# Performance work log

Hardware: AMD Instinct MI355X
Metric: run time of the kernel (lower is better)

## Reference

```python
import jax, jax.numpy as jnp
import numpy as np

N, E, F_IN = 50000, 800000, 64
HID, HEADS = 64, 4
NEG_SLOPE = 0.2  # PyG GATConv default leaky_relu slope
BN_EPS = 1e-5
NEG_BIG = -1e9
# (in_dim, heads, out_per_head) for each of the 3 layers
DIMS = [(F_IN, HEADS, HID), (HID * HEADS, HEADS, HID), (HID * HEADS, 1, 2)]


def setup_inputs() -> dict:
    key = jax.random.key(0)
    kx, ke, ka, kp = jax.random.split(key, 4)
    inp = {
        "x": jax.random.normal(kx, (N, F_IN), jnp.float32),
        "edge_index": jax.random.randint(ke, (2, E), 0, N),
        "edge_attr": jax.random.randint(ka, (E, 1), 0, 4),
    }
    pk = jax.random.split(kp, 6 * len(DIMS))
    c = 0
    for i, (din, h, dout) in enumerate(DIMS):
        # 4 edge-type-specific GAT convs, params stacked along leading axis
        inp[f"W{i}"] = jax.random.normal(pk[c], (4, din, h * dout), jnp.float32) / np.float32(np.sqrt(din)); c += 1
        inp[f"As{i}"] = jax.random.normal(pk[c], (4, h, dout), jnp.float32) * 0.1; c += 1
        inp[f"Ad{i}"] = jax.random.normal(pk[c], (4, h, dout), jnp.float32) * 0.1; c += 1
        inp[f"cb{i}"] = jnp.zeros((4, h * dout), jnp.float32)
        inp[f"skW{i}"] = jax.random.normal(pk[c], (din, h * dout), jnp.float32) / np.float32(np.sqrt(din)); c += 1
        inp[f"skb{i}"] = jnp.zeros((h * dout,), jnp.float32)
        inp[f"bng{i}"] = jnp.ones((din,), jnp.float32)
        inp[f"bnb{i}"] = jnp.zeros((din,), jnp.float32)
    return inp


def batch_norm(x, gamma, beta):
    # training-mode BatchNorm1d over the node axis (biased variance, as in torch)
    m = x.mean(axis=0)
    v = x.var(axis=0)
    return (x - m) * jax.lax.rsqrt(v + BN_EPS) * gamma + beta


def gat_conv(x, W, a_src, a_dst, bias, src, dst, mask, n):
    # Standard GAT attention restricted to edges of one class (mask) --
    # equivalent to running the conv on the boolean-indexed subgraph.
    heads, dout = a_src.shape
    h = (x @ W).reshape(n, heads, dout)                      # [N,H,D]
    es = jnp.einsum('nhd,hd->nh', h, a_src)                  # [N,H]
    ed = jnp.einsum('nhd,hd->nh', h, a_dst)                  # [N,H]
    e = jax.nn.leaky_relu(es[src] + ed[dst], NEG_SLOPE)      # [E,H]
    e = jnp.where(mask[:, None], e, NEG_BIG)
    emax = jax.ops.segment_max(e, dst, num_segments=n)       # [N,H]
    emax = jnp.where(jnp.isfinite(emax), emax, 0.0)          # empty segments -> -inf
    a = jnp.exp(e - emax[dst])
    a = jnp.where(mask[:, None], a, 0.0)
    denom = jax.ops.segment_sum(a, dst, num_segments=n)      # [N,H]
    msg = jax.ops.segment_sum(a[:, :, None] * h[src], dst, num_segments=n)  # [N,H,D]
    out = msg / jnp.where(denom > 0, denom, 1.0)[:, :, None]
    return out.reshape(n, heads * dout) + bias


def reference(x, edge_index, edge_attr,
              W0, As0, Ad0, cb0, skW0, skb0, bng0, bnb0,
              W1, As1, Ad1, cb1, skW1, skb1, bng1, bnb1,
              W2, As2, Ad2, cb2, skW2, skb2, bng2, bnb2):
    src, dst = edge_index[0], edge_index[1]
    edge_class = edge_attr[:, -1]
    n = x.shape[0]
    layers = [
        (W0, As0, Ad0, cb0, skW0, skb0, bng0, bnb0),
        (W1, As1, Ad1, cb1, skW1, skb1, bng1, bnb1),
        (W2, As2, Ad2, cb2, skW2, skb2, bng2, bnb2),
    ]
    for (W, As, Ad, cb, skW, skb, g, b) in layers:
        x = batch_norm(x, g, b)
        x0 = x @ skW + skb
        for j in range(4):  # fixed small loop over edge types
            x0 = x0 + gat_conv(x, W[j], As[j], Ad[j], cb[j], src, dst,
                               edge_class == j, n)
        x = jax.nn.relu(x0)
    return x
```

## Files before the change

kernel.cpp:

```cpp
#include <hip/hip_runtime.h>
#include <cstddef>
#include <cstdint>

#define NN 50000
#define EE 800000

constexpr float BN_EPS   = 1e-5f;
constexpr float NEGSLOPE = 0.2f;

typedef short s16x8 __attribute__((ext_vector_type(8)));
typedef float f32x4 __attribute__((ext_vector_type(4)));
typedef unsigned short u16x4 __attribute__((ext_vector_type(4)));

__device__ __forceinline__ unsigned short f2bf(float f) {
  unsigned int u = __float_as_uint(f);
  unsigned int r = (u + 0x7fffu + ((u >> 16) & 1u)) >> 16;
  return (unsigned short)r;
}
__device__ __forceinline__ float bf2f(unsigned short u) {
  return __uint_as_float(((unsigned int)u) << 16);
}
__device__ __forceinline__ float leaky(float e) { return e >= 0.f ? e : NEGSLOPE * e; }
__device__ __forceinline__ float sel4(float v0, float v1, float v2, float v3, int h) {
  float r = v0;
  r = (h == 1) ? v1 : r;
  r = (h == 2) ? v2 : r;
  r = (h == 3) ? v3 : r;
  return r;
}
__device__ __forceinline__ void gl_lds16(const unsigned short* g, unsigned short* l) {
  __builtin_amdgcn_global_load_lds(
      (const __attribute__((address_space(1))) unsigned int*)(g),
      (__attribute__((address_space(3))) unsigned int*)(l), 16, 0, 0);
}

__global__ void count_edges_k(const int* __restrict__ ei, const int* __restrict__ cls,
                              int* __restrict__ counts) {
  int e = blockIdx.x * 256 + threadIdx.x;
  if (e >= EE) return;
  int dst = ei[EE + e];
  int c   = cls[e];
  atomicAdd(&counts[dst * 4 + c], 1);
}

__global__ void scan_local_k(const int* __restrict__ counts, int* __restrict__ rs,
                             int* __restrict__ bsum, int n) {
  __shared__ int sh[256];
  int b = blockIdx.x, t = threadIdx.x;
  int base = b * 1024;
  int v[4];
  #pragma unroll
  for (int q = 0; q < 4; q++) {
    int i = base + t * 4 + q;
    v[q] = (i < n) ? counts[i] : 0;
  }
  v[1] += v[0]; v[2] += v[1]; v[3] += v[2];
  sh[t] = v[3];
  __syncthreads();
  for (int off = 1; off < 256; off <<= 1) {
    int x = (t >= off) ? sh[t - off] : 0;
    __syncthreads();
    sh[t] += x;
    __syncthreads();
  }
  int prev = (t > 0) ? sh[t - 1] : 0;
  #pragma unroll
  for (int q = 0; q < 4; q++) {
    int i = base + t * 4 + q;
    if (i < n) rs[i + 1] = prev + v[q];
  }
  if (t == 255) bsum[b] = sh[255];
}

__global__ void scan_bsum_k(int* __restrict__ bsum, int nb) {
  __shared__ int sh[256];
  int t = threadIdx.x;
  sh[t] = (t < nb) ? bsum[t] : 0;
  __syncthreads();
  for (int off = 1; off < 256; off <<= 1) {
    int x = (t >= off) ? sh[t - off] : 0;
    __syncthreads();
    sh[t] += x;
    __syncthreads();
  }
  if (t < nb) bsum[t] = (t > 0) ? sh[t - 1] : 0;
}

__global__ void scan_add_k(int* __restrict__ rs, const int* __restrict__ bsum, int n) {
  int b = blockIdx.x, t = threadIdx.x;
  int off = bsum[b];
  #pragma unroll
  for (int q = 0; q < 4; q++) {
    int i = b * 1024 + t * 4 + q;
    if (i < n) rs[i + 1] += off;
  }
  if (b == 0 && t == 0) rs[0] = 0;
}

__global__ void fill_edges_k(const int* __restrict__ ei, const int* __restrict__ cls,
                             const int* __restrict__ rs, int* __restrict__ cursor,
                             int* __restrict__ ssrc) {
  int e = blockIdx.x * 256 + threadIdx.x;
  if (e >= EE) return;
  int dst = ei[EE + e];
  int c   = cls[e];
  int bin = dst * 4 + c;
  int pos = rs[bin] + atomicAdd(&cursor[bin], 1);
  ssrc[pos] = ei[e];
}

template <bool RELU>
__global__ void bn_stats_k(const float* __restrict__ x, float* __restrict__ sums,
                           int din, int total4) {
  __shared__ float ls[512];
  int t = threadIdx.x;
  for (int i = t; i < 2 * din; i += 256) ls[i] = 0.f;
  __syncthreads();
  int dmask = din - 1;
  int start = blockIdx.x * 256 + t;
  int c0 = (start * 4) & dmask;
  float s[4] = {0.f, 0.f, 0.f, 0.f};
  float ss[4] = {0.f, 0.f, 0.f, 0.f};
  for (int idx = start; idx < total4; idx += gridDim.x * 256) {
    float4 v = ((const float4*)x)[idx];
    float a0 = RELU ? fmaxf(v.x, 0.f) : v.x;
    float a1 = RELU ? fmaxf(v.y, 0.f) : v.y;
    float a2 = RELU ? fmaxf(v.z, 0.f) : v.z;
    float a3 = RELU ? fmaxf(v.w, 0.f) : v.w;
    s[0] += a0; s[1] += a1; s[2] += a2; s[3] += a3;
    ss[0] += a0 * a0; ss[1] += a1 * a1; ss[2] += a2 * a2; ss[3] += a3 * a3;
  }
  #pragma unroll
  for (int q = 0; q < 4; q++) {
    atomicAdd(&ls[c0 + q], s[q]);
    atomicAdd(&ls[din + c0 + q], ss[q]);
  }
  __syncthreads();
  for (int i = t; i < 2 * din; i += 256) atomicAdd(&sums[i], ls[i]);
}

__global__ void bn_finalize_k(const float* __restrict__ sums, const float* __restrict__ g,
                              const float* __restrict__ b, float* __restrict__ scale,
                              float* __restrict__ shift, int din,
                              const float* __restrict__ skb, const float* __restrict__ cb,
                              float* __restrict__ skbe, int hd) {
  int i = threadIdx.x;
  if (i < din) {
    float m  = sums[i] / (float)NN;
    float v  = sums[din + i] / (float)NN - m * m;
    float r  = rsqrtf(v + BN_EPS);
    float sc = r * g[i];
    scale[i] = sc;
    shift[i] = b[i] - m * sc;
  }
  if (i < hd) {
    float acc = skb[i];
    #pragma unroll
    for (int j = 0; j < 4; j++) acc += cb[j * hd + i];
    skbe[i] = acc;
  }
}

template <bool RELU>
__global__ void bn_apply_bf16_k(const float* __restrict__ x, unsigned short* __restrict__ xn,
                                const float* __restrict__ scale, const float* __restrict__ shift,
                                int dmask, int total4) {
  for (int i = blockIdx.x * 256 + threadIdx.x; i < total4; i += gridDim.x * 256) {
    float4 v = ((const float4*)x)[i];
    int c0 = (i * 4) & dmask;
    if (RELU) {
      v.x = fmaxf(v.x, 0.f); v.y = fmaxf(v.y, 0.f);
      v.z = fmaxf(v.z, 0.f); v.w = fmaxf(v.w, 0.f);
    }
    u16x4 o;
    o[0] = f2bf(v.x * scale[c0 + 0] + shift[c0 + 0]);
    o[1] = f2bf(v.y * scale[c0 + 1] + shift[c0 + 1]);
    o[2] = f2bf(v.z * scale[c0 + 2] + shift[c0 + 2]);
    o[3] = f2bf(v.w * scale[c0 + 3] + shift[c0 + 3]);
    ((u16x4*)xn)[i] = o;
  }
}

__global__ void conv_weights_k(const float* __restrict__ skW0, const float* __restrict__ W0,
                               const float* __restrict__ skW1, const float* __restrict__ W1,
                               unsigned short* __restrict__ wt) {
  int o = blockIdx.x * 256 + threadIdx.x;
  if (o >= 409600) return;
  float v;
  if (o < 16384) {
    int n = o >> 6, k = o & 63;
    v = skW0[k * 256 + n];
  } else if (o < 81920) {
    int w = o - 16384; int j = w >> 14; w &= 16383;
    int n = w >> 6, k = w & 63;
    v = W0[j * 16384 + k * 256 + n];
  } else if (o < 147456) {
    int w = o - 81920;
    int n = w >> 8, k = w & 255;
    v = skW1[k * 256 + n];
  } else {
    int w = o - 147456; int j = w >> 16; w &= 65535;
    int n = w >> 8, k = w & 255;
    v = W1[j * 65536 + k * 256 + n];
  }
  wt[o] = f2bf(v);
}

__global__ __launch_bounds__(256) void gemm_bf16_k(
    const unsigned short* __restrict__ A,
    const unsigned short* __restrict__ Bt,
    const float* __restrict__ bias,
    float* __restrict__ Cf,
    unsigned short* __restrict__ Cb,
    const float* __restrict__ asrc,
    const float* __restrict__ adst,
    float* __restrict__ es4,
    float* __restrict__ ed4,
    int M, int K, int N, int strideBt, long long strideC) {
  __shared__ unsigned short As[128 * 32];
  __shared__ unsigned short Bs[128 * 32];
  int z = blockIdx.z;
  Bt += (size_t)z * strideBt;
  int tid  = threadIdx.x;
  int lane = tid & 63;
  int w    = tid >> 6;
  int lm = lane & 15, lq = lane >> 4;
  int row0 = blockIdx.y * 128, col0 = blockIdx.x * 128;
  int wr = (w >> 1) * 64, wc = (w & 1) * 64;
  f32x4 acc[4][4];
  #pragma unroll
  for (int i = 0; i < 4; i++)
    #pragma unroll
    for (int j = 0; j < 4; j++) acc[i][j] = {0.f, 0.f, 0.f, 0.f};
  int ldsbase = (tid & ~63) * 16;

  for (int k0 = 0; k0 < K; k0 += 32) {
    #pragma unroll
    for (int r = 0; r < 2; r++) {
      int ia = r * 256 + tid;
      int arow = row0 + (ia >> 2);
      if (arow >= M) arow = M - 1;
      const unsigned short* ga = A + (size_t)arow * K + k0 + (ia & 3) * 8;
      gl_lds16(ga, (unsigned short*)((char*)As + r * 4096 + ldsbase));
      int bcol = col0 + (ia >> 2);
      const unsigned short* gb = Bt + (size_t)bcol * K + k0 + (ia & 3) * 8;
      gl_lds16(gb, (unsigned short*)((char*)Bs + r * 4096 + ldsbase));
    }
    __syncthreads();
    s16x8 af[4], bfr[4];
    #pragma unroll
    for (int i = 0; i < 4; i++)
      af[i] = *(const s16x8*)&As[(wr + i * 16 + lm) * 32 + lq * 8];
    #pragma unroll
    for (int j = 0; j < 4; j++)
      bfr[j] = *(const s16x8*)&Bs[(wc + j * 16 + lm) * 32 + lq * 8];
    #pragma unroll
    for (int i = 0; i < 4; i++)
      #pragma unroll
      for (int j = 0; j < 4; j++)
        acc[i][j] = __builtin_amdgcn_mfma_f32_16x16x32_bf16(af[i], bfr[j], acc[i][j], 0, 0, 0);
    __syncthreads();
  }

  #pragma unroll
  for (int i = 0; i < 4; i++) {
    #pragma unroll
    for (int j = 0; j < 4; j++) {
      int c = col0 + wc + j * 16 + lm;
      #pragma unroll
      for (int rg = 0; rg < 4; rg++) {
        int r = row0 + wr + i * 16 + lq * 4 + rg;
        if (r < M) {
          float v = acc[i][j][rg];
          if (Cf) {
            if (bias) v += bias[c];
            Cf[(size_t)r * N + c] = v;
          } else {
            Cb[(size_t)z * strideC + (size_t)r * N + c] = f2bf(v);
          }
        }
      }
    }
  }

  if (es4) {
    int hh = (col0 + wc) >> 6;
    float as_v[4], ad_v[4];
    #pragma unroll
    for (int j = 0; j < 4; j++) {
      int gcol = col0 + wc + j * 16 + lm;
      as_v[j] = asrc[z * 256 + gcol];
      ad_v[j] = adst[z * 256 + gcol];
    }
    #pragma unroll
    for (int i = 0; i < 4; i++) {
      #pragma unroll
      for (int rg = 0; rg < 4; rg++) {
        float se = 0.f, sd = 0.f;
        #pragma unroll
        for (int j = 0; j < 4; j++) {
          se += acc[i][j][rg] * as_v[j];
          sd += acc[i][j][rg] * ad_v[j];
        }
        #pragma unroll
        for (int off = 8; off > 0; off >>= 1) {
          se += __shfl_xor(se, off);
          sd += __shfl_xor(sd, off);
        }
        int r = row0 + wr + i * 16 + lq * 4 + rg;
        if (r < M) {
          if (lm == 0) es4[((size_t)z * NN + r) * 4 + hh] = se;
          if (lm == 1) ed4[((size_t)z * NN + r) * 4 + hh] = sd;
        }
      }
    }
  }
}

__global__ __launch_bounds__(256) void gat_agg4_fused_k(
    const unsigned short* __restrict__ hfeat4,
    const float* __restrict__ es4,
    const float* __restrict__ ed4,
    const int* __restrict__ rs, const int* __restrict__ ssrc,
    float* __restrict__ x0) {
  int node = blockIdx.x * 4 + (threadIdx.x >> 6);
  int lane = threadIdx.x & 63;
  if (node >= NN) return;
  int r0 = rs[node * 4 + 0], r1 = rs[node * 4 + 1], r2 = rs[node * 4 + 2],
      r3 = rs[node * 4 + 3], r4 = rs[node * 4 + 4];
  if (r0 == r4) return;
  int h = lane >> 4;

  float acc[4][4];
  float den[4];
  #pragma unroll
  for (int j = 0; j < 4; j++) {
    den[j] = 0.f;
    #pragma unroll
    for (int q = 0; q < 4; q++) acc[j][q] = 0.f;
  }

  #pragma unroll
  for (int j = 0; j < 4; j++) {
    int beg = (j == 0) ? r0 : (j == 1) ? r1 : (j == 2) ? r2 : r3;
    int end = (j == 0) ? r1 : (j == 1) ? r2 : (j == 2) ? r3 : r4;
    if (beg == end) continue;
    const float4 edv = *(const float4*)(ed4 + ((size_t)j * NN + node) * 4);
    const unsigned short* hfj = hfeat4 + (size_t)j * NN * 256;
    const float* esj = es4 + (size_t)j * NN * 4;
    for (int base = beg; base < end; base += 64) {
      int idx = base + lane;
      int s = -1;
      float w0 = 0.f, w1 = 0.f, w2 = 0.f, w3 = 0.f;
      if (idx < end) {
        s = ssrc[idx];
        float4 ev = *(const float4*)(esj + (size_t)s * 4);
        w0 = __expf(leaky(ev.x + edv.x));
        w1 = __expf(leaky(ev.y + edv.y));
        w2 = __expf(leaky(ev.z + edv.z));
        w3 = __expf(leaky(ev.w + edv.w));
      }
      int n_e = min(64, end - base);
      #pragma unroll 2
      for (int i = 0; i < n_e; i++) {
        int si   = __shfl(s, i);
        float b0 = __shfl(w0, i), b1 = __shfl(w1, i),
              b2 = __shfl(w2, i), b3 = __shfl(w3, i);
        float wh = sel4(b0, b1, b2, b3, h);
        u16x4 f = *(const u16x4*)(hfj + (size_t)si * 256 + lane * 4);
        acc[j][0] += wh * bf2f(f[0]);
        acc[j][1] += wh * bf2f(f[1]);
        acc[j][2] += wh * bf2f(f[2]);
        acc[j][3] += wh * bf2f(f[3]);
        den[j] += wh;
      }
    }
  }

  float4* xp = (float4*)(x0 + (size_t)node * 256 + lane * 4);
  float4 cur = *xp;
  #pragma unroll
  for (int j = 0; j < 4; j++) {
    if (den[j] > 0.f) {
      float inv = 1.f / den[j];
      cur.x += acc[j][0] * inv;
      cur.y += acc[j][1] * inv;
      cur.z += acc[j][2] * inv;
      cur.w += acc[j][3] * inv;
    }
  }
  *xp = cur;
}

__global__ __launch_bounds__(256) void layer2_fused_k(
    const unsigned short* __restrict__ xa,
    const float* __restrict__ skW,
    const float* __restrict__ W,
    const float* __restrict__ As2,
    const float* __restrict__ Ad2,
    const float* __restrict__ skbe,
    float* __restrict__ x02,
    float* __restrict__ hf2,
    float* __restrict__ es2,
    float* __restrict__ ed2) {
  __shared__ float wsk[256][2];
  __shared__ float wcl[4][256][2];
  int t = threadIdx.x;
  wsk[t][0] = skW[t * 2];
  wsk[t][1] = skW[t * 2 + 1];
  #pragma unroll
  for (int j = 0; j < 4; j++) {
    wcl[j][t][0] = W[j * 512 + t * 2];
    wcl[j][t][1] = W[j * 512 + t * 2 + 1];
  }
  __syncthreads();
  int node = blockIdx.x * 256 + t;
  if (node >= NN) return;
  const unsigned short* row = xa + (size_t)node * 256;
  float s0 = 0.f, s1 = 0.f;
  float h[4][2] = {};
  for (int k = 0; k < 256; k += 4) {
    u16x4 xr = *(const u16x4*)(row + k);
    #pragma unroll
    for (int q = 0; q < 4; q++) {
      float xv = bf2f(xr[q]);
      s0 += xv * wsk[k + q][0];
      s1 += xv * wsk[k + q][1];
      #pragma unroll
      for (int j = 0; j < 4; j++) {
        h[j][0] += xv * wcl[j][k + q][0];
        h[j][1] += xv * wcl[j][k + q][1];
      }
    }
  }
  x02[(size_t)node * 2]     = s0 + skbe[0];
  x02[(size_t)node * 2 + 1] = s1 + skbe[1];
  #pragma unroll
  for (int j = 0; j < 4; j++) {
    hf2[((size_t)j * NN + node) * 2]     = h[j][0];
    hf2[((size_t)j * NN + node) * 2 + 1] = h[j][1];
    es2[(size_t)j * NN + node] = h[j][0] * As2[j * 2] + h[j][1] * As2[j * 2 + 1];
    ed2[(size_t)j * NN + node] = h[j][0] * Ad2[j * 2] + h[j][1] * Ad2[j * 2 + 1];
  }
}

__global__ __launch_bounds__(256) void gat_agg2_fused_k(
    const float* __restrict__ hf2,
    const float* __restrict__ es2,
    const float* __restrict__ ed2,
    const int* __restrict__ rs, const int* __restrict__ ssrc,
    float* __restrict__ x0) {
  int node = blockIdx.x * 4 + (threadIdx.x >> 6);
  int lane = threadIdx.x & 63;
  if (node >= NN) return;
  float add0 = 0.f, add1 = 0.f;
  #pragma unroll
  for (int j = 0; j < 4; j++) {
    int beg = rs[node * 4 + j], end = rs[node * 4 + j + 1];
    if (beg == end) continue;
    float edv = ed2[(size_t)j * NN + node];
    float nw = 0.f, n0 = 0.f, n1 = 0.f;
    for (int idx = beg + lane; idx < end; idx += 64) {
      int s = ssrc[idx];
      float w = __expf(leaky(es2[(size_t)j * NN + s] + edv));
      float2 f = *(const float2*)(hf2 + ((size_t)j * NN + s) * 2);
      nw += w; n0 += w * f.x; n1 += w * f.y;
    }
    #pragma unroll
    for (int off = 32; off > 0; off >>= 1) {
      nw += __shfl_xor(nw, off);
      n0 += __shfl_xor(n0, off);
      n1 += __shfl_xor(n1, off);
    }
    float inv = 1.f / nw;
    add0 += n0 * inv;
    add1 += n1 * inv;
  }
  if (lane == 0) {
    x0[(size_t)node * 2]     += add0;
    x0[(size_t)node * 2 + 1] += add1;
  }
}

__global__ void relu_k(const float* __restrict__ in, float* __restrict__ out, int n) {
  for (int i = blockIdx.x * 256 + threadIdx.x; i < n; i += gridDim.x * 256)
    out[i] = fmaxf(in[i], 0.f);
}

extern "C" void kernel_launch(void* const* d_in, const int* in_sizes, int n_in,
                              void* d_out, int out_size, void* d_ws, size_t ws_size,
                              hipStream_t stream) {
  (void)in_sizes; (void)n_in; (void)out_size; (void)ws_size;
  const float* x_in = (const float*)d_in[0];
  const int* ei  = (const int*)d_in[1];
  const int* cls = (const int*)d_in[2];
  const float *W[3], *Asr[3], *Adr[3], *cb[3], *skW[3], *skb[3], *bng[3], *bnb[3];
  for (int i = 0; i < 3; i++) {
    int b = 3 + 8 * i;
    W[i]   = (const float*)d_in[b + 0];
    Asr[i] = (const float*)d_in[b + 1];
    Adr[i] = (const float*)d_in[b + 2];
    cb[i]  = (const float*)d_in[b + 3];
    skW[i] = (const float*)d_in[b + 4];
    skb[i] = (const float*)d_in[b + 5];
    bng[i] = (const float*)d_in[b + 6];
    bnb[i] = (const float*)d_in[b + 7];
  }
  float* out = (float*)d_out;

  char* wsp = (char*)d_ws;
  auto alloc = [&](size_t bytes) {
    char* p = wsp;
    wsp += (bytes + 255) & ~(size_t)255;
    return p;
  };
  float*          x0     = (float*)alloc((size_t)NN * 256 * 4);
  unsigned short* xa     = (unsigned short*)alloc((size_t)NN * 256 * 2);
  unsigned short* hfeat4 = (unsigned short*)alloc((size_t)4 * NN * 256 * 2);
  float*          hf2    = (float*)alloc((size_t)4 * NN * 2 * 4);
  float*          es4    = (float*)alloc((size_t)4 * NN * 4 * 4);
  float*          ed4    = (float*)alloc((size_t)4 * NN * 4 * 4);
  float*          stats  = (float*)alloc(512 * 4);
  float*          scale  = (float*)alloc(256 * 4);
  float*          shift  = (float*)alloc(256 * 4);
  float*          skbe   = (float*)alloc(256 * 4);
  unsigned short* wt     = (unsigned short*)alloc((size_t)409600 * 2);
  int*            counts = (int*)alloc((size_t)NN * 4 * 4);
  int*            rs     = (int*)alloc(((size_t)NN * 4 + 1) * 4);
  int*            cursor = (int*)alloc((size_t)NN * 4 * 4);
  int*            bsum   = (int*)alloc(256 * 4);
  int*            ssrc   = (int*)alloc((size_t)EE * 4);

  hipMemsetAsync(counts, 0, (size_t)NN * 4 * 4, stream);
  hipMemsetAsync(cursor, 0, (size_t)NN * 4 * 4, stream);
  count_edges_k<<<(EE + 255) / 256, 256, 0, stream>>>(ei, cls, counts);
  scan_local_k<<<196, 256, 0, stream>>>(counts, rs, bsum, NN * 4);
  scan_bsum_k<<<1, 256, 0, stream>>>(bsum, 196);
  scan_add_k<<<196, 256, 0, stream>>>(rs, bsum, NN * 4);
  fill_edges_k<<<(EE + 255) / 256, 256, 0, stream>>>(ei, cls, rs, cursor, ssrc);

  conv_weights_k<<<1600, 256, 0, stream>>>(skW[0], W[0], skW[1], W[1], wt);

  for (int L = 0; L < 2; L++) {
    int din = (L == 0) ? 64 : 256;
    int total4 = NN * din / 4;
    const float* lin = (L == 0) ? x_in : x0;
    hipMemsetAsync(stats, 0, 512 * 4, stream);
    if (L == 0) {
      bn_stats_k<false><<<512, 256, 0, stream>>>(lin, stats, din, total4);
    } else {
      bn_stats_k<true><<<512, 256, 0, stream>>>(lin, stats, din, total4);
    }
    bn_finalize_k<<<1, 256, 0, stream>>>(stats, bng[L], bnb[L], scale, shift, din,
                                         skb[L], cb[L], skbe, 256);
    if (L == 0) {
      bn_apply_bf16_k<false><<<1024, 256, 0, stream>>>(lin, xa, scale, shift, din - 1, total4);
    } else {
      bn_apply_bf16_k<true><<<1024, 256, 0, stream>>>(lin, xa, scale, shift, din - 1, total4);
    }

    const unsigned short* wsk = wt + (L ? 81920 : 0);
    dim3 ggs(2, (NN + 127) / 128, 1);
    gemm_bf16_k<<<ggs, 256, 0, stream>>>(xa, wsk, skbe, x0, nullptr,
                                         nullptr, nullptr, nullptr, nullptr,
                                         NN, din, 256, 0, 0);
    const unsigned short* wcv = wt + (L ? 147456 : 16384);
    int sB = L ? 65536 : 16384;
    dim3 ggc(2, (NN + 127) / 128, 4);
    gemm_bf16_k<<<ggc, 256, 0, stream>>>(xa, wcv, nullptr, nullptr, hfeat4,
                                         Asr[L], Adr[L], es4, ed4,
                                         NN, din, 256, sB, (long long)NN * 256);
    gat_agg4_fused_k<<<(NN + 3) / 4, 256, 0, stream>>>(hfeat4, es4, ed4, rs, ssrc, x0);
  }

  hipMemsetAsync(stats, 0, 512 * 4, stream);
  bn_stats_k<true><<<512, 256, 0, stream>>>(x0, stats, 256, NN * 64);
  bn_finalize_k<<<1, 256, 0, stream>>>(stats, bng[2], bnb[2], scale, shift, 256,
                                       skb[2], cb[2], skbe, 2);
  bn_apply_bf16_k<true><<<1024, 256, 0, stream>>>(x0, xa, scale, shift, 255, NN * 64);
  layer2_fused_k<<<(NN + 255) / 256, 256, 0, stream>>>(xa, skW[2], W[2], Asr[2], Adr[2],
                                                       skbe, x0, hf2, es4, ed4);
  gat_agg2_fused_k<<<(NN + 3) / 4, 256, 0, stream>>>(hf2, es4, ed4, rs, ssrc, x0);
  relu_k<<<64, 256, 0, stream>>>(x0, out, NN * 2);
}
```

Measured before the change: 758.9 us.

## Merge skip and conv GEMMs, single-pass aggregation for low-degree nodes, fuse final relu

The skip GEMM and the four per-class conv GEMMs now run as one launch with a five-slice grid. The layer-0/1 aggregation kernel gains a fast path for nodes with at most 64 incoming edges. That path computes all edge weights at once, normalises them per class with a wave prefix scan, stages them in LDS, and then runs one gather loop over all classes instead of four serial loops. The last aggregation writes relu(x02 + msg) directly, which removes the separate relu kernel. The intent is to cut launch count, tail effects and per-class loop overhead, at the cost of more complex code and extra shuffles.

Result: faster. 692.2 us (-8.8%).

```diff
diff --git a/kernel.cpp b/kernel.cpp
--- a/kernel.cpp
+++ b/kernel.cpp
@@ -208,19 +208,20 @@
 
 __global__ __launch_bounds__(256) void gemm_bf16_k(
     const unsigned short* __restrict__ A,
-    const unsigned short* __restrict__ Bt,
-    const float* __restrict__ bias,
-    float* __restrict__ Cf,
-    unsigned short* __restrict__ Cb,
+    const unsigned short* __restrict__ BtSk,
+    const unsigned short* __restrict__ BtCv,
+    const float* __restrict__ skbe,
+    float* __restrict__ x0,
+    unsigned short* __restrict__ hfeat4,
     const float* __restrict__ asrc,
     const float* __restrict__ adst,
     float* __restrict__ es4,
     float* __restrict__ ed4,
-    int M, int K, int N, int strideBt, long long strideC) {
+    int M, int K) {
   __shared__ unsigned short As[128 * 32];
   __shared__ unsigned short Bs[128 * 32];
   int z = blockIdx.z;
-  Bt += (size_t)z * strideBt;
+  const unsigned short* Bt = (z == 0) ? BtSk : BtCv + (size_t)(z - 1) * 256 * K;
   int tid  = threadIdx.x;
   int lane = tid & 63;
   int w    = tid >> 6;
@@ -262,35 +263,39 @@
     __syncthreads();
   }
 
-  #pragma unroll
-  for (int i = 0; i < 4; i++) {
-    #pragma unroll
-    for (int j = 0; j < 4; j++) {
-      int c = col0 + wc + j * 16 + lm;
+  if (z == 0) {
+    #pragma unroll
+    for (int i = 0; i < 4; i++)
       #pragma unroll
-      for (int rg = 0; rg < 4; rg++) {
-        int r = row0 + wr + i * 16 + lq * 4 + rg;
-        if (r < M) {
-          float v = acc[i][j][rg];
-          if (Cf) {
-            if (bias) v += bias[c];
-            Cf[(size_t)r * N + c] = v;
-          } else {
-            Cb[(size_t)z * strideC + (size_t)r * N + c] = f2bf(v);
-          }
+      for (int j = 0; j < 4; j++) {
+        int c = col0 + wc + j * 16 + lm;
+        #pragma unroll
+        for (int rg = 0; rg < 4; rg++) {
+          int r = row0 + wr + i * 16 + lq * 4 + rg;
+          if (r < M) x0[(size_t)r * 256 + c] = acc[i][j][rg] + skbe[c];
         }
       }
-    }
-  }
-
-  if (es4) {
+  } else {
+    int cl = z - 1;
+    unsigned short* Cb = hfeat4 + (size_t)cl * NN * 256;
+    #pragma unroll
+    for (int i = 0; i < 4; i++)
+      #pragma unroll
+      for (int j = 0; j < 4; j++) {
+        int c = col0 + wc + j * 16 + lm;
+        #pragma unroll
+        for (int rg = 0; rg < 4; rg++) {
+          int r = row0 + wr + i * 16 + lq * 4 + rg;
+          if (r < M) Cb[(size_t)r * 256 + c] = f2bf(acc[i][j][rg]);
+        }
+      }
     int hh = (col0 + wc) >> 6;
     float as_v[4], ad_v[4];
     #pragma unroll
     for (int j = 0; j < 4; j++) {
       int gcol = col0 + wc + j * 16 + lm;
-      as_v[j] = asrc[z * 256 + gcol];
-      ad_v[j] = adst[z * 256 + gcol];
+      as_v[j] = asrc[cl * 256 + gcol];
+      ad_v[j] = adst[cl * 256 + gcol];
     }
     #pragma unroll
     for (int i = 0; i < 4; i++) {
@@ -309,8 +314,8 @@
         }
         int r = row0 + wr + i * 16 + lq * 4 + rg;
         if (r < M) {
-          if (lm == 0) es4[((size_t)z * NN + r) * 4 + hh] = se;
-          if (lm == 1) ed4[((size_t)z * NN + r) * 4 + hh] = sd;
+          if (lm == 0) es4[((size_t)cl * NN + r) * 4 + hh] = se;
+          if (lm == 1) ed4[((size_t)cl * NN + r) * 4 + hh] = sd;
         }
       }
     }
@@ -323,72 +328,112 @@
     const float* __restrict__ ed4,
     const int* __restrict__ rs, const int* __restrict__ ssrc,
     float* __restrict__ x0) {
-  int node = blockIdx.x * 4 + (threadIdx.x >> 6);
+  __shared__ float aw[4][256];
+  int wv   = threadIdx.x >> 6;
+  int node = blockIdx.x * 4 + wv;
   int lane = threadIdx.x & 63;
   if (node >= NN) return;
   int r0 = rs[node * 4 + 0], r1 = rs[node * 4 + 1], r2 = rs[node * 4 + 2],
       r3 = rs[node * 4 + 3], r4 = rs[node * 4 + 4];
-  if (r0 == r4) return;
-  int h = lane >> 4;
-
-  float acc[4][4];
-  float den[4];
-  #pragma unroll
-  for (int j = 0; j < 4; j++) {
-    den[j] = 0.f;
-    #pragma unroll
-    for (int q = 0; q < 4; q++) acc[j][q] = 0.f;
-  }
-
-  #pragma unroll
-  for (int j = 0; j < 4; j++) {
-    int beg = (j == 0) ? r0 : (j == 1) ? r1 : (j == 2) ? r2 : r3;
-    int end = (j == 0) ? r1 : (j == 1) ? r2 : (j == 2) ? r3 : r4;
-    if (beg == end) continue;
-    const float4 edv = *(const float4*)(ed4 + ((size_t)j * NN + node) * 4);
-    const unsigned short* hfj = hfeat4 + (size_t)j * NN * 256;
-    const float* esj = es4 + (size_t)j * NN * 4;
-    for (int base = beg; base < end; base += 64) {
-      int idx = base + lane;
-      int s = -1;
-      float w0 = 0.f, w1 = 0.f, w2 = 0.f, w3 = 0.f;
-      if (idx < end) {
-        s = ssrc[idx];
-        float4 ev = *(const float4*)(esj + (size_t)s * 4);
-        w0 = __expf(leaky(ev.x + edv.x));
-        w1 = __expf(leaky(ev.y + edv.y));
-        w2 = __expf(leaky(ev.z + edv.z));
-        w3 = __expf(leaky(ev.w + edv.w));
+  int En = r4 - r0;
+  if (En == 0) return;
+  int hd = lane >> 4;
+  float acc0 = 0.f, acc1 = 0.f, acc2 = 0.f, acc3 = 0.f;
+
+  if (En <= 64) {
+    int idx = r0 + lane;
+    bool valid = idx < r4;
+    int j = 0, ri = 0;
+    float w0 = 0.f, w1 = 0.f, w2 = 0.f, w3 = 0.f;
+    if (valid) {
+      j = (idx >= r1) + (idx >= r2) + (idx >= r3);
+      int s = ssrc[idx];
+      ri = j * NN + s;
+      float4 ev = *(const float4*)(es4 + (size_t)ri * 4);
+      float4 dv = *(const float4*)(ed4 + ((size_t)j * NN + node) * 4);
+      w0 = __expf(leaky(ev.x + dv.x));
+      w1 = __expf(leaky(ev.y + dv.y));
+      w2 = __expf(leaky(ev.z + dv.z));
+      w3 = __expf(leaky(ev.w + dv.w));
+    }
+    float p0 = w0, p1 = w1, p2 = w2, p3 = w3;
+    #pragma unroll
+    for (int off = 1; off < 64; off <<= 1) {
+      float t0 = __shfl_up(p0, off), t1 = __shfl_up(p1, off);
+      float t2 = __shfl_up(p2, off), t3 = __shfl_up(p3, off);
+      if (lane >= off) { p0 += t0; p1 += t1; p2 += t2; p3 += t3; }
+    }
+    if (valid) {
+      int b1 = r1 - r0, b2 = r2 - r0, b3 = r3 - r0, b4 = r4 - r0;
+      int endl = sel4((float)b1, (float)b2, (float)b3, (float)b4, j);
+      int begl = sel4(0.f, (float)b1, (float)b2, (float)b3, j);
+      int ei2 = (int)endl - 1;
+      int bi2 = (int)begl - 1;
+      float d0 = __shfl(p0, ei2), d1 = __shfl(p1, ei2);
+      float d2 = __shfl(p2, ei2), d3 = __shfl(p3, ei2);
+      float q0 = __shfl(p0, bi2 < 0 ? 0 : bi2), q1 = __shfl(p1, bi2 < 0 ? 0 : bi2);
+      float q2 = __shfl(p2, bi2 < 0 ? 0 : bi2), q3 = __shfl(p3, bi2 < 0 ? 0 : bi2);
+      if (bi2 < 0) { q0 = 0.f; q1 = 0.f; q2 = 0.f; q3 = 0.f; }
+      w0 /= (d0 - q0); w1 /= (d1 - q1); w2 /= (d2 - q2); w3 /= (d3 - q3);
+    } else {
+      w0 = w1 = w2 = w3 = 0.f;
+    }
+    *(float4*)&aw[wv][lane * 4] = make_float4(w0, w1, w2, w3);
+    __builtin_amdgcn_s_waitcnt(0);
+    #pragma unroll 2
+    for (int i = 0; i < En; i++) {
+      int rib = __shfl(ri, i);
+      float a = aw[wv][i * 4 + hd];
+      u16x4 f = *(const u16x4*)(hfeat4 + ((size_t)rib << 8) + lane * 4);
+      acc0 += a * bf2f(f[0]);
+      acc1 += a * bf2f(f[1]);
+      acc2 += a * bf2f(f[2]);
+      acc3 += a * bf2f(f[3]);
+    }
+  } else {
+    #pragma unroll
+    for (int j = 0; j < 4; j++) {
+      int beg = (j == 0) ? r0 : (j == 1) ? r1 : (j == 2) ? r2 : r3;
+      int end = (j == 0) ? r1 : (j == 1) ? r2 : (j == 2) ? r3 : r4;
+      if (beg == end) continue;
+      float4 edv = *(const float4*)(ed4 + ((size_t)j * NN + node) * 4);
+      const float* esj = es4 + (size_t)j * NN * 4;
+      const unsigned short* hfj = hfeat4 + (size_t)j * NN * 256;
+      float n0 = 0.f, n1 = 0.f, n2 = 0.f, n3 = 0.f, den = 0.f;
+      for (int b2 = beg; b2 < end; b2 += 64) {
+        int idx = b2 + lane;
+        int s = 0;
+        float w0 = 0.f, w1 = 0.f, w2 = 0.f, w3 = 0.f;
+        if (idx < end) {
+          s = ssrc[idx];
+          float4 ev = *(const float4*)(esj + (size_t)s * 4);
+          w0 = __expf(leaky(ev.x + edv.x));
+          w1 = __expf(leaky(ev.y + edv.y));
+          w2 = __expf(leaky(ev.z + edv.z));
+          w3 = __expf(leaky(ev.w + edv.w));
+        }
+        int n_e = min(64, end - b2);
+        for (int i = 0; i < n_e; i++) {
+          int si = __shfl(s, i);
+          float c0 = __shfl(w0, i), c1 = __shfl(w1, i),
+                c2 = __shfl(w2, i), c3 = __shfl(w3, i);
+          float wh = sel4(c0, c1, c2, c3, hd);
+          u16x4 f = *(const u16x4*)(hfj + (size_t)si * 256 + lane * 4);
+          n0 += wh * bf2f(f[0]);
+          n1 += wh * bf2f(f[1]);
+          n2 += wh * bf2f(f[2]);
+          n3 += wh * bf2f(f[3]);
+          den += wh;
+        }
       }
-      int n_e = min(64, end - base);
-      #pragma unroll 2
-      for (int i = 0; i < n_e; i++) {
-        int si   = __shfl(s, i);
-        float b0 = __shfl(w0, i), b1 = __shfl(w1, i),
-              b2 = __shfl(w2, i), b3 = __shfl(w3, i);
-        float wh = sel4(b0, b1, b2, b3, h);
-        u16x4 f = *(const u16x4*)(hfj + (size_t)si * 256 + lane * 4);
-        acc[j][0] += wh * bf2f(f[0]);
-        acc[j][1] += wh * bf2f(f[1]);
-        acc[j][2] += wh * bf2f(f[2]);
-        acc[j][3] += wh * bf2f(f[3]);
-        den[j] += wh;
-      }
+      float inv = 1.f / den;
+      acc0 += n0 * inv; acc1 += n1 * inv; acc2 += n2 * inv; acc3 += n3 * inv;
     }
   }
 
   float4* xp = (float4*)(x0 + (size_t)node * 256 + lane * 4);
   float4 cur = *xp;
-  #pragma unroll
-  for (int j = 0; j < 4; j++) {
-    if (den[j] > 0.f) {
-      float inv = 1.f / den[j];
-      cur.x += acc[j][0] * inv;
-      cur.y += acc[j][1] * inv;
-      cur.z += acc[j][2] * inv;
-      cur.w += acc[j][3] * inv;
-    }
-  }
+  cur.x += acc0; cur.y += acc1; cur.z += acc2; cur.w += acc3;
   *xp = cur;
 }
 
@@ -449,7 +494,8 @@
     const float* __restrict__ es2,
     const float* __restrict__ ed2,
     const int* __restrict__ rs, const int* __restrict__ ssrc,
-    float* __restrict__ x0) {
+    const float* __restrict__ x02,
+    float* __restrict__ out) {
   int node = blockIdx.x * 4 + (threadIdx.x >> 6);
   int lane = threadIdx.x & 63;
   if (node >= NN) return;
@@ -477,14 +523,9 @@
     add1 += n1 * inv;
   }
   if (lane == 0) {
-    x0[(size_t)node * 2]     += add0;
-    x0[(size_t)node * 2 + 1] += add1;
-  }
-}
-
-__global__ void relu_k(const float* __restrict__ in, float* __restrict__ out, int n) {
-  for (int i = blockIdx.x * 256 + threadIdx.x; i < n; i += gridDim.x * 256)
-    out[i] = fmaxf(in[i], 0.f);
+    out[(size_t)node * 2]     = fmaxf(x02[(size_t)node * 2] + add0, 0.f);
+    out[(size_t)node * 2 + 1] = fmaxf(x02[(size_t)node * 2 + 1] + add1, 0.f);
+  }
 }
 
 extern "C" void kernel_launch(void* const* d_in, const int* in_sizes, int n_in,
@@ -520,6 +561,7 @@
   float*          hf2    = (float*)alloc((size_t)4 * NN * 2 * 4);
   float*          es4    = (float*)alloc((size_t)4 * NN * 4 * 4);
   float*          ed4    = (float*)alloc((size_t)4 * NN * 4 * 4);
+  float*          x02    = (float*)alloc((size_t)NN * 2 * 4);
   float*          stats  = (float*)alloc(512 * 4);
   float*          scale  = (float*)alloc(256 * 4);
   float*          shift  = (float*)alloc(256 * 4);
@@ -560,16 +602,10 @@
     }
 
     const unsigned short* wsk = wt + (L ? 81920 : 0);
-    dim3 ggs(2, (NN + 127) / 128, 1);
-    gemm_bf16_k<<<ggs, 256, 0, stream>>>(xa, wsk, skbe, x0, nullptr,
-                                         nullptr, nullptr, nullptr, nullptr,
-                                         NN, din, 256, 0, 0);
     const unsigned short* wcv = wt + (L ? 147456 : 16384);
-    int sB = L ? 65536 : 16384;
-    dim3 ggc(2, (NN + 127) / 128, 4);
-    gemm_bf16_k<<<ggc, 256, 0, stream>>>(xa, wcv, nullptr, nullptr, hfeat4,
-                                         Asr[L], Adr[L], es4, ed4,
-                                         NN, din, 256, sB, (long long)NN * 256);
+    dim3 gg(2, (NN + 127) / 128, 5);
+    gemm_bf16_k<<<gg, 256, 0, stream>>>(xa, wsk, wcv, skbe, x0, hfeat4,
+                                        Asr[L], Adr[L], es4, ed4, NN, din);
     gat_agg4_fused_k<<<(NN + 3) / 4, 256, 0, stream>>>(hfeat4, es4, ed4, rs, ssrc, x0);
   }
 
@@ -579,7 +615,6 @@
                                        skb[2], cb[2], skbe, 2);
   bn_apply_bf16_k<true><<<1024, 256, 0, stream>>>(x0, xa, scale, shift, 255, NN * 64);
   layer2_fused_k<<<(NN + 255) / 256, 256, 0, stream>>>(xa, skW[2], W[2], Asr[2], Adr[2],
-                                                       skbe, x0, hf2, es4, ed4);
-  gat_agg2_fused_k<<<(NN + 3) / 4, 256, 0, stream>>>(hf2, es4, ed4, rs, ssrc, x0);
-  relu_k<<<64, 256, 0, stream>>>(x0, out, NN * 2);
-}
+                                                       skbe, x02, hf2, es4, ed4);
+  gat_agg2_fused_k<<<(NN + 3) / 4, 256, 0, stream>>>(hf2, es4, ed4, rs, ssrc, x02, out);
+}
```
